# Performance work log

Measured on AMD Instinct MI355X. Metric: run time of the kernel, lower is better.

The kernel has to match this reference:

```python
import jax, jax.numpy as jnp
import numpy as np

BBOX_POS_MAX = 1024.0
BN_EPS = 1e-5


def _bn_eval(x, g, b, rm, rv):
    # BatchNorm1d in eval mode: affine transform with running stats
    return g * (x - rm) * jax.lax.rsqrt(rv + BN_EPS) + b


def setup_inputs() -> dict:
    key = jax.random.key(0)
    ks = jax.random.split(key, 24)
    B, N, F = 32, 512, 1024
    E = 32768
    H1, H2, H3 = 512, 256, 128          # node_pred_hidden
    EH1, EH2 = 64, 64                   # edge_pred_hidden
    NC, EC = 8, 10                      # node/edge concept channels
    BC = 9                              # bbox_channels (4 bbox + 4 dir + 1 prio)
    s = 0.02
    inp = {
        'roi_features': jax.random.normal(ks[0], (B, N, F), jnp.float32),
        'batch_bboxes': jax.random.uniform(ks[1], (B, N, 4), jnp.float32) * BBOX_POS_MAX,
        'batch_directions': jax.random.uniform(ks[2], (B, N, 4), jnp.float32),
        'batch_priorities': jax.random.uniform(ks[3], (B, N), jnp.float32),
        'batch_edge_index': jax.random.randint(ks[4], (B, 2, E), 0, N, jnp.int32),
        # node_predictor params
        'np_w1': jax.random.normal(ks[5], (F, H1), jnp.float32) * s,
        'np_b1': jnp.zeros((H1,), jnp.float32),
        'bn1_g': jnp.ones((H1,), jnp.float32),
        'bn1_b': jnp.zeros((H1,), jnp.float32),
        'bn1_rm': jnp.zeros((H1,), jnp.float32),
        'bn1_rv': jnp.ones((H1,), jnp.float32),
        'np_w2': jax.random.normal(ks[6], (H1, H2), jnp.float32) * s,
        'np_b2': jnp.zeros((H2,), jnp.float32),
        'bn2_g': jnp.ones((H2,), jnp.float32),
        'bn2_b': jnp.zeros((H2,), jnp.float32),
        'bn2_rm': jnp.zeros((H2,), jnp.float32),
        'bn2_rv': jnp.ones((H2,), jnp.float32),
        'np_w3': jax.random.normal(ks[7], (H2, H3), jnp.float32) * s,
        'np_b3': jnp.zeros((H3,), jnp.float32),
        'ni_w': jax.random.normal(ks[8], (H3, NC), jnp.float32) * s,
        'ni_b': jnp.zeros((NC,), jnp.float32),
        # edge_predictor params (input dim = 2 * bbox_channels)
        'ep_w1': jax.random.normal(ks[9], (2 * BC, EH1), jnp.float32) * s,
        'ep_b1': jnp.zeros((EH1,), jnp.float32),
        'ep_w2': jax.random.normal(ks[10], (EH1, EH2), jnp.float32) * s,
        'ep_b2': jnp.zeros((EH2,), jnp.float32),
        'ei_w': jax.random.normal(ks[11], (EH2, EC), jnp.float32) * s,
        'ei_b': jnp.zeros((EC,), jnp.float32),
    }
    return inp


def reference(roi_features, batch_bboxes, batch_directions, batch_priorities,
              batch_edge_index,
              np_w1, np_b1, bn1_g, bn1_b, bn1_rm, bn1_rv,
              np_w2, np_b2, bn2_g, bn2_b, bn2_rm, bn2_rv,
              np_w3, np_b3, ni_w, ni_b,
              ep_w1, ep_b1, ep_w2, ep_b2, ei_w, ei_b):
    B, N, F = roi_features.shape
    # ---- node path: MLP (eval-mode BN, dropout = identity) + sigmoid interpreter
    x = roi_features.reshape(B * N, F)
    h = jax.nn.relu(_bn_eval(x @ np_w1 + np_b1, bn1_g, bn1_b, bn1_rm, bn1_rv))
    h = jax.nn.relu(_bn_eval(h @ np_w2 + np_b2, bn2_g, bn2_b, bn2_rm, bn2_rv))
    h = jax.nn.relu(h @ np_w3 + np_b3)
    node_concepts = jax.nn.sigmoid(h @ ni_w + ni_b).reshape(B, N, -1)
    # ---- edge path: per-batch gather of node attrs via edge_index, concat, MLP
    node_attr = jnp.concatenate(
        [batch_bboxes / BBOX_POS_MAX, batch_directions, batch_priorities[..., None]],
        axis=-1)  # [B, N, 9]
    C = node_attr.shape[-1]
    src_idx = batch_edge_index[:, 0, :, None]  # [B, E, 1]
    dst_idx = batch_edge_index[:, 1, :, None]
    src = jnp.take_along_axis(node_attr, src_idx.astype(jnp.int32), axis=1)  # [B, E, 9]
    dst = jnp.take_along_axis(node_attr, dst_idx.astype(jnp.int32), axis=1)
    edge_attr = jnp.concatenate([src, dst], axis=-1).reshape(-1, 2 * C)  # [B*E, 18]
    e = jax.nn.relu(edge_attr @ ep_w1 + ep_b1)
    e = jax.nn.relu(e @ ep_w2 + ep_b2)
    edge_concepts = jax.nn.sigmoid(e @ ei_w + ei_b)  # [B*E, EC]
    return node_concepts, edge_concepts
```

## Files before the change

kernel.cpp:

```cpp
#include <hip/hip_runtime.h>
#include <cstdint>
#include <cstddef>

#define BN_EPSF 1e-5f

constexpr int B_  = 32, N_ = 512, F_ = 1024, E_ = 32768;
constexpr int H1_ = 512, H2_ = 256, H3_ = 128, NC_ = 8, EC_ = 10;
constexpr int M_  = B_ * N_;
constexpr int NE_ = B_ * E_;

typedef short bf16x8 __attribute__((ext_vector_type(8)));
typedef float f32x4  __attribute__((ext_vector_type(4)));

__device__ __forceinline__ short f2bf(float f) {
  union { float f; unsigned u; } v; v.f = f;
  unsigned r = v.u + 0x7fffu + ((v.u >> 16) & 1u);
  return (short)(r >> 16);
}
__device__ __forceinline__ unsigned cvtpk(float a, float b) {
  unsigned r;
  asm("v_cvt_pk_bf16_f32 %0, %1, %2" : "=v"(r) : "v"(a), "v"(b));
  return r;
}

#define GLDS(gp, lp) __builtin_amdgcn_global_load_lds( \
    (const __attribute__((address_space(1))) void*)(gp), \
    (__attribute__((address_space(3))) void*)(lp), 16, 0, 0)

#define MFMA(a, b, c) __builtin_amdgcn_mfma_f32_16x16x32_bf16((a), (b), (c), 0, 0, 0)

__device__ __forceinline__ void wt_body(
    const float* __restrict__ W, short* __restrict__ Wt, int K, int N,
    int bx, int by, float (*s)[33])
{
  const int tx = threadIdx.x & 31, ty = threadIdx.x >> 5;
  const int k0 = by * 32, n0 = bx * 32;
#pragma unroll
  for (int r = 0; r < 4; r++)
    s[ty * 4 + r][tx] = W[(size_t)(k0 + ty * 4 + r) * N + n0 + tx];
  __syncthreads();
#pragma unroll
  for (int r = 0; r < 4; r++)
    Wt[(size_t)(n0 + ty * 4 + r) * K + k0 + tx] = f2bf(s[tx][ty * 4 + r]);
}

__global__ __launch_bounds__(256) void k_prep(
    const float* __restrict__ roi, ushort* __restrict__ roiB,
    const float* __restrict__ w1, short* __restrict__ w1t,
    const float* __restrict__ w2, short* __restrict__ w2t,
    const float* __restrict__ w3, short* __restrict__ w3t)
{
  __shared__ float s[32][33];
  const int bx = blockIdx.x;
  if (bx < 8192) {
    int i = bx * 256 + threadIdx.x;
    float4 a = *(const float4*)(roi + (size_t)i * 8);
    float4 b = *(const float4*)(roi + (size_t)i * 8 + 4);
    unsigned o[4];
    o[0] = cvtpk(a.x, a.y); o[1] = cvtpk(a.z, a.w);
    o[2] = cvtpk(b.x, b.y); o[3] = cvtpk(b.z, b.w);
    *(uint4*)(roiB + (size_t)i * 8) = *(uint4*)o;
  } else if (bx < 8704) {
    int idx = bx - 8192; wt_body(w1, w1t, F_, H1_, idx & 15, idx >> 4, s);
  } else if (bx < 8832) {
    int idx = bx - 8704; wt_body(w2, w2t, H1_, H2_, idx & 7, idx >> 3, s);
  } else {
    int idx = bx - 8832; wt_body(w3, w3t, H2_, H3_, idx & 3, idx >> 2, s);
  }
}

__device__ __forceinline__ void relu_pack_shuf(
    const f32x4 (&acc)[4], int la, int lb, bool lo32, bf16x8 (&out)[2])
{
  unsigned plo[4], phi[4];
#pragma unroll
  for (int t = 0; t < 4; t++) {
    plo[t] = cvtpk(fmaxf(acc[t][0], 0.f), fmaxf(acc[t][1], 0.f));
    phi[t] = cvtpk(fmaxf(acc[t][2], 0.f), fmaxf(acc[t][3], 0.f));
  }
#pragma unroll
  for (int ks = 0; ks < 2; ks++) {
    unsigned w0a = (unsigned)__shfl((int)plo[2 * ks], la);
    unsigned w0b = (unsigned)__shfl((int)plo[2 * ks + 1], la);
    unsigned w1a = (unsigned)__shfl((int)phi[2 * ks], la);
    unsigned w1b = (unsigned)__shfl((int)phi[2 * ks + 1], la);
    unsigned w2a = (unsigned)__shfl((int)plo[2 * ks], lb);
    unsigned w2b = (unsigned)__shfl((int)plo[2 * ks + 1], lb);
    unsigned w3a = (unsigned)__shfl((int)phi[2 * ks], lb);
    unsigned w3b = (unsigned)__shfl((int)phi[2 * ks + 1], lb);
    union { unsigned u[4]; bf16x8 v; } t;
    t.u[0] = lo32 ? w0a : w0b;
    t.u[1] = lo32 ? w1a : w1b;
    t.u[2] = lo32 ? w2a : w2b;
    t.u[3] = lo32 ? w3a : w3b;
    out[ks] = t.v;
  }
}

__global__ __launch_bounds__(256, 3) void k_fused(
    const float* __restrict__ bbox, const float* __restrict__ dir,
    const float* __restrict__ pri, const int* __restrict__ eidx,
    const float* __restrict__ ew1, const float* __restrict__ eb1,
    const float* __restrict__ ew2, const float* __restrict__ eb2,
    const float* __restrict__ eow, const float* __restrict__ eob,
    float* __restrict__ out_edge,
    const short* __restrict__ roiB, const short* __restrict__ w1t,
    const float* __restrict__ b1, const float* __restrict__ g1,
    const float* __restrict__ bb1, const float* __restrict__ rm1,
    const float* __restrict__ rv1, short* __restrict__ h1)
{
  __shared__ __align__(16) char arena[38912];

  const int bx = blockIdx.x;
  const int rsel = bx % 3;
  const int tid  = threadIdx.x;
  const int wave = tid >> 6, lane = tid & 63;
  const int lm = lane & 15;

  if (rsel == 2) {
    const int lb = bx / 3;
    short* As = (short*)arena;
    short* Bs = (short*)(arena + 16384);
    const int m0 = (lb >> 2) * 128, n0 = (lb & 3) * 128;
    const int wm = wave >> 1, wn = wave & 1;
    const int q  = lane >> 4;
    const int srow = tid >> 3;
    const int sko  = ((tid & 7) ^ (srow & 7)) * 8;

    f32x4 acc[4][4] = {};
    for (int k0 = 0; k0 < F_; k0 += 64) {
#pragma unroll
      for (int it = 0; it < 4; it++)
        GLDS(roiB + (size_t)(m0 + it * 32 + srow) * F_ + k0 + sko,
             (char*)As + it * 4096 + wave * 1024);
#pragma unroll
      for (int it = 0; it < 4; it++)
        GLDS(w1t + (size_t)(n0 + it * 32 + srow) * F_ + k0 + sko,
             (char*)Bs + it * 4096 + wave * 1024);
      __syncthreads();

#pragma unroll
      for (int ks = 0; ks < 2; ks++) {
        const int co = (((ks * 4 + q) ^ (lm & 7)) * 8);
        bf16x8 af[4], bfr[4];
#pragma unroll
        for (int t = 0; t < 4; t++) {
          af[t]  = *(const bf16x8*)&As[(wm * 64 + t * 16 + lm) * 64 + co];
          bfr[t] = *(const bf16x8*)&Bs[(wn * 64 + t * 16 + lm) * 64 + co];
        }
#pragma unroll
        for (int ti = 0; ti < 4; ti++)
#pragma unroll
          for (int tj = 0; tj < 4; tj++)
            acc[ti][tj] = MFMA(af[ti], bfr[tj], acc[ti][tj]);
      }
      __syncthreads();
    }
#pragma unroll
    for (int tj = 0; tj < 4; tj++) {
      const int col = n0 + wn * 64 + tj * 16 + lm;
      const float bi = b1[col];
      float s = g1[col] * rsqrtf(rv1[col] + BN_EPSF);
      float t = bb1[col] - rm1[col] * s;
#pragma unroll
      for (int ti = 0; ti < 4; ti++) {
        const int rbase = m0 + wm * 64 + ti * 16 + ((lane >> 4) << 2);
#pragma unroll
        for (int r = 0; r < 4; r += 2) {
          float va = fmaf(acc[ti][tj][r]     + bi, s, t);
          float vb = fmaf(acc[ti][tj][r + 1] + bi, s, t);
          unsigned p = cvtpk(fmaxf(va, 0.f), fmaxf(vb, 0.f));
          h1[(size_t)(rbase + r)     * H1_ + col] = (short)p;
          h1[(size_t)(rbase + r + 1) * H1_ + col] = (short)(p >> 16);
        }
      }
    }
    return;
  }

  const int eb    = (bx / 3) * 2 + rsel;
  const int batch = eb >> 5;
  const int q     = lane >> 4;

  short*  sW1   = (short*)arena;
  short*  sW2   = (short*)(arena + 4096);
  short*  sW3   = (short*)(arena + 12288);
  ushort* sAttr = (ushort*)(arena + 14336);

  for (int i = tid; i < 2048; i += 256) {
    int n = i >> 5, k = i & 31;
    short v = 0;
    if (k < 9)                  v = f2bf(ew1[k * 64 + n]);
    else if (k >= 16 && k < 25) v = f2bf(ew1[(k - 7) * 64 + n]);
    sW1[i] = v;
  }
  for (int i = tid; i < 4096; i += 256) {
    int n = i >> 6, k = i & 63;
    sW2[i] = f2bf(ew2[k * 64 + n]);
  }
  for (int i = tid; i < 1024; i += 256) {
    int n = i >> 6, k = i & 63;
    sW3[i] = (n < 10) ? f2bf(eow[k * 10 + n]) : (short)0;
  }
  {
    const float inv = 1.0f / 1024.0f;
    for (int n = tid; n < 512; n += 256) {
      int gi = batch * 512 + n;
      float4 bv = *(const float4*)(bbox + (size_t)gi * 4);
      float4 dv = *(const float4*)(dir + (size_t)gi * 4);
      float pp = pri[gi];
      uint4 lo, hi;
      lo.x = cvtpk(bv.x * inv, bv.y * inv); lo.y = cvtpk(bv.z * inv, bv.w * inv);
      lo.z = cvtpk(dv.x, dv.y);             lo.w = cvtpk(dv.z, dv.w);
      hi.x = cvtpk(pp, 0.f); hi.y = 0; hi.z = 0; hi.w = 0;
      *(uint4*)&sAttr[n * 24]     = lo;
      *(uint4*)&sAttr[n * 24 + 8] = hi;
    }
  }
  __syncthreads();

  bf16x8 fW1[4], fW2[4][2], fW3[2];
#pragma unroll
  for (int t = 0; t < 4; t++)
    fW1[t] = *(const bf16x8*)&sW1[(t * 16 + lm) * 32 + q * 8];
#pragma unroll
  for (int t = 0; t < 4; t++)
#pragma unroll
    for (int ks = 0; ks < 2; ks++)
      fW2[t][ks] = *(const bf16x8*)&sW2[(t * 16 + lm) * 64 + ks * 32 + q * 8];
#pragma unroll
  for (int ks = 0; ks < 2; ks++)
    fW3[ks] = *(const bf16x8*)&sW3[lm * 64 + ks * 32 + q * 8];

  f32x4 b1q[4], b2q[4], boq;
#pragma unroll
  for (int t = 0; t < 4; t++) {
    b1q[t] = *(const f32x4*)(eb1 + t * 16 + q * 4);
    b2q[t] = *(const f32x4*)(eb2 + t * 16 + q * 4);
  }
#pragma unroll
  for (int r = 0; r < 4; r++)
    boq[r] = (q * 4 + r < 10) ? eob[q * 4 + r] : 0.f;

  const int  la   = (lane & 15) | ((lane & 16) << 1);
  const int  lbn  = la + 16;
  const bool lo32 = (lane < 32);
  const int* ip   = eidx + (size_t)batch * 2 * E_ + ((lane >= 32) ? E_ : 0);
  const int  ebl  = (eb & 31) * 1024;
  const int  ah   = (lane & 16) ? 8 : 0;

  int nidx[8][2];
#pragma unroll
  for (int b = 0; b < 8; b++)
#pragma unroll
    for (int ti = 0; ti < 2; ti++)
      nidx[b][ti] = ip[ebl + b * 128 + wave * 32 + ti * 16 + lm];

  bf16x8 xf[2];
#pragma unroll
  for (int ti = 0; ti < 2; ti++)
    xf[ti] = *(const bf16x8*)&sAttr[nidx[0][ti] * 24 + ah];

#pragma unroll
  for (int bi = 0; bi < 8; bi++) {
    bf16x8 xn[2];
    if (bi < 7) {
#pragma unroll
      for (int ti = 0; ti < 2; ti++)
        xn[ti] = *(const bf16x8*)&sAttr[nidx[bi + 1][ti] * 24 + ah];
    }

    f32x4 acc1[2][4];
#pragma unroll
    for (int tj = 0; tj < 4; tj++)
#pragma unroll
      for (int ti = 0; ti < 2; ti++)
        acc1[ti][tj] = MFMA(fW1[tj], xf[ti], b1q[tj]);
    bf16x8 xf2[2][2];
#pragma unroll
    for (int ti = 0; ti < 2; ti++)
      relu_pack_shuf(acc1[ti], la, lbn, lo32, xf2[ti]);

    f32x4 acc2[2][4];
#pragma unroll
    for (int ti = 0; ti < 2; ti++)
#pragma unroll
      for (int tj = 0; tj < 4; tj++)
        acc2[ti][tj] = b2q[tj];
#pragma unroll
    for (int ks = 0; ks < 2; ks++)
#pragma unroll
      for (int tj = 0; tj < 4; tj++)
#pragma unroll
        for (int ti = 0; ti < 2; ti++)
          acc2[ti][tj] = MFMA(fW2[tj][ks], xf2[ti][ks], acc2[ti][tj]);
    bf16x8 xf3[2][2];
#pragma unroll
    for (int ti = 0; ti < 2; ti++)
      relu_pack_shuf(acc2[ti], la, lbn, lo32, xf3[ti]);

#pragma unroll
    for (int ti = 0; ti < 2; ti++) {
      f32x4 a3 = boq;
#pragma unroll
      for (int ks = 0; ks < 2; ks++)
        a3 = MFMA(fW3[ks], xf3[ti][ks], a3);
      float o[4];
#pragma unroll
      for (int r = 0; r < 4; r++)
        o[r] = 1.f / (1.f + __expf(-a3[r]));
      size_t base = (size_t)(eb * 1024 + bi * 128 + wave * 32 + ti * 16 + lm) * 10;
      if (q == 0) {
        float2 t0; t0.x = o[0]; t0.y = o[1]; *(float2*)(out_edge + base)     = t0;
        float2 t1; t1.x = o[2]; t1.y = o[3]; *(float2*)(out_edge + base + 2) = t1;
      } else if (q == 1) {
        float2 t0; t0.x = o[0]; t0.y = o[1]; *(float2*)(out_edge + base + 4) = t0;
        float2 t1; t1.x = o[2]; t1.y = o[3]; *(float2*)(out_edge + base + 6) = t1;
      } else if (q == 2) {
        float2 t0; t0.x = o[0]; t0.y = o[1]; *(float2*)(out_edge + base + 8) = t0;
      }
    }
    xf[0] = xn[0]; xf[1] = xn[1];
  }
}

__global__ __launch_bounds__(256) void k_tail(
    const short* __restrict__ h1, const short* __restrict__ w2t,
    const short* __restrict__ w3t,
    const float* __restrict__ b2, const float* __restrict__ g2,
    const float* __restrict__ bb2, const float* __restrict__ rm2,
    const float* __restrict__ rv2,
    const float* __restrict__ b3, const float* __restrict__ niw,
    const float* __restrict__ nib, float* __restrict__ out)
{
  __shared__ __align__(16) char arena[53760];
  short* sA  = (short*)arena;
  short* sB  = (short*)(arena + 4096);
  short* sH2 = (short*)(arena + 36864);
  short* sB3 = (short*)arena;
  short* sH3 = (short*)(arena + 16384);

  const int tid  = threadIdx.x;
  const int wave = tid >> 6, lane = tid & 63;
  const int lm = lane & 15, q = lane >> 4;
  const int wm = wave >> 1, wn = wave & 1;
  const int m0 = blockIdx.x * 32;
  const int srow = tid >> 2;
  const int skq  = ((tid & 3) ^ ((tid >> 3) & 3)) * 8;
  const int sq   = (q ^ ((lm >> 1) & 3)) * 8;

  f32x4 acc2[8] = {};
  for (int k0 = 0; k0 < 512; k0 += 64) {
    {
      int c = tid >> 7, row = (tid >> 2) & 31;
      GLDS(h1 + (size_t)(m0 + row) * 512 + k0 + c * 32 + skq,
           (char*)sA + wave * 1024);
    }
#pragma unroll
    for (int it = 0; it < 4; it++)
#pragma unroll
      for (int c = 0; c < 2; c++)
        GLDS(w2t + (size_t)(it * 64 + srow) * 512 + k0 + c * 32 + skq,
             (char*)sB + c * 16384 + it * 4096 + wave * 1024);
    __syncthreads();
#pragma unroll
    for (int c = 0; c < 2; c++) {
      bf16x8 af = *(const bf16x8*)&sA[c * 1024 + (wm * 16 + lm) * 32 + sq];
#pragma unroll
      for (int nt = 0; nt < 8; nt++) {
        bf16x8 bfr = *(const bf16x8*)&sB[c * 8192 + (wn * 128 + nt * 16 + lm) * 32 + sq];
        acc2[nt] = MFMA(af, bfr, acc2[nt]);
      }
    }
    __syncthreads();
  }
#pragma unroll
  for (int nt = 0; nt < 8; nt++) {
    int col = wn * 128 + nt * 16 + lm;
    float s = g2[col] * rsqrtf(rv2[col] + BN_EPSF);
    float t = bb2[col] - rm2[col] * s;
    float bi = b2[col];
    float v0 = fmaf(acc2[nt][0] + bi, s, t);
    float v1 = fmaf(acc2[nt][1] + bi, s, t);
    float v2 = fmaf(acc2[nt][2] + bi, s, t);
    float v3 = fmaf(acc2[nt][3] + bi, s, t);
    unsigned p01 = cvtpk(fmaxf(v0, 0.f), fmaxf(v1, 0.f));
    unsigned p23 = cvtpk(fmaxf(v2, 0.f), fmaxf(v3, 0.f));
    int rb = wm * 16 + q * 4;
    sH2[(rb + 0) * 264 + col] = (short)p01;
    sH2[(rb + 1) * 264 + col] = (short)(p01 >> 16);
    sH2[(rb + 2) * 264 + col] = (short)p23;
    sH2[(rb + 3) * 264 + col] = (short)(p23 >> 16);
  }
  __syncthreads();

  f32x4 acc3[4] = {};
  for (int k0 = 0; k0 < 256; k0 += 64) {
#pragma unroll
    for (int it = 0; it < 2; it++)
#pragma unroll
      for (int c = 0; c < 2; c++)
        GLDS(w3t + (size_t)(it * 64 + srow) * 256 + k0 + c * 32 + skq,
             (char*)sB3 + c * 8192 + it * 4096 + wave * 1024);
    __syncthreads();
#pragma unroll
    for (int c = 0; c < 2; c++) {
      bf16x8 af = *(const bf16x8*)&sH2[(wm * 16 + lm) * 264 + k0 + c * 32 + q * 8];
#pragma unroll
      for (int nt = 0; nt < 4; nt++) {
        bf16x8 bfr = *(const bf16x8*)&sB3[c * 4096 + (wn * 64 + nt * 16 + lm) * 32 + sq];
        acc3[nt] = MFMA(af, bfr, acc3[nt]);
      }
    }
    __syncthreads();
  }
#pragma unroll
  for (int nt = 0; nt < 4; nt++) {
    int col = wn * 64 + nt * 16 + lm;
    float bi = b3[col];
    float v0 = acc3[nt][0] + bi;
    float v1 = acc3[nt][1] + bi;
    float v2 = acc3[nt][2] + bi;
    float v3 = acc3[nt][3] + bi;
    unsigned p01 = cvtpk(fmaxf(v0, 0.f), fmaxf(v1, 0.f));
    unsigned p23 = cvtpk(fmaxf(v2, 0.f), fmaxf(v3, 0.f));
    int rb = wm * 16 + q * 4;
    sH3[(rb + 0) * 136 + col] = (short)p01;
    sH3[(rb + 1) * 136 + col] = (short)(p01 >> 16);
    sH3[(rb + 2) * 136 + col] = (short)p23;
    sH3[(rb + 3) * 136 + col] = (short)(p23 >> 16);
  }
  __syncthreads();

  if (wave < 2) {
    f32x4 a4 = {};
#pragma unroll
    for (int c = 0; c < 4; c++) {
      ushort tmp[8];
#pragma unroll
      for (int j = 0; j < 8; j++) {
        int k = c * 32 + q * 8 + j;
        tmp[j] = (lm < 8) ? (ushort)f2bf(niw[k * 8 + lm]) : (ushort)0;
      }
      bf16x8 fw = *(bf16x8*)tmp;
      bf16x8 af4 = *(const bf16x8*)&sH3[(wave * 16 + lm) * 136 + c * 32 + q * 8];
      a4 = MFMA(af4, fw, a4);
    }
    if (lm < 8) {
      float bi = nib[lm];
#pragma unroll
      for (int r = 0; r < 4; r++) {
        float v = a4[r] + bi;
        out[(size_t)(m0 + wave * 16 + q * 4 + r) * 8 + lm] = 1.f / (1.f + __expf(-v));
      }
    }
  }
}

extern "C" void kernel_launch(void* const* d_in, const int* in_sizes, int n_in,
                              void* d_out, int out_size, void* d_ws, size_t ws_size,
                              hipStream_t stream)
{
  const float* roi   = (const float*)d_in[0];
  const float* bbox  = (const float*)d_in[1];
  const float* dir   = (const float*)d_in[2];
  const float* pri   = (const float*)d_in[3];
  const int*   eidx  = (const int*)d_in[4];
  const float* w1    = (const float*)d_in[5];
  const float* b1    = (const float*)d_in[6];
  const float* g1    = (const float*)d_in[7];
  const float* bb1   = (const float*)d_in[8];
  const float* rm1   = (const float*)d_in[9];
  const float* rv1   = (const float*)d_in[10];
  const float* w2    = (const float*)d_in[11];
  const float* b2    = (const float*)d_in[12];
  const float* g2    = (const float*)d_in[13];
  const float* bb2   = (const float*)d_in[14];
  const float* rm2   = (const float*)d_in[15];
  const float* rv2   = (const float*)d_in[16];
  const float* w3    = (const float*)d_in[17];
  const float* b3    = (const float*)d_in[18];
  const float* niw   = (const float*)d_in[19];
  const float* nib   = (const float*)d_in[20];
  const float* ew1   = (const float*)d_in[21];
  const float* eb1   = (const float*)d_in[22];
  const float* ew2   = (const float*)d_in[23];
  const float* eb2   = (const float*)d_in[24];
  const float* eow   = (const float*)d_in[25];
  const float* eob   = (const float*)d_in[26];

  float* out_node = (float*)d_out;
  float* out_edge = (float*)d_out + (size_t)M_ * NC_;

  char* w = (char*)d_ws;
  short*  roiB = (short*)w;
  short*  w1t  = (short*)(w + 33554432);
  short*  w2t  = (short*)(w + 34603008);
  short*  w3t  = (short*)(w + 34865152);
  short*  h1   = (short*)(w + 35717120);

  k_prep<<<8864, 256, 0, stream>>>(roi, (ushort*)roiB, w1, w1t, w2, w2t,
                                   w3, w3t);

  k_fused<<<1536, 256, 0, stream>>>(
      bbox, dir, pri, eidx, ew1, eb1, ew2, eb2, eow, eob, out_edge,
      roiB, w1t, b1, g1, bb1, rm1, rv1, h1);

  k_tail<<<M_ / 32, 256, 0, stream>>>(
      h1, w2t, w3t, b2, g2, bb2, rm2, rv2, b3, niw, nib, out_node);
}
```

Measured before the change: 237.9 us.

## Precompute bf16 node attrs in prep and double-buffer tail GEMM staging

Node attribute packing (bbox scaling, directions, priority to bf16) moves from every edge block into the prep kernel, which writes a global table. Edge blocks now gather the attributes straight from global memory instead of staging them in LDS, which shrinks their LDS footprint. The tail kernel's layer-2 and layer-3 GEMMs switch to double-buffered LDS staging so the next K-tile loads overlap the current MFMAs. The cost is more LDS in the tail kernel (72KB), which may reduce its occupancy, and edge gathers that now go to global/L2 instead of LDS.

Measured after the change: 239.4 us. About the same (+0.6%).

```diff
diff --git a/kernel.cpp b/kernel.cpp
--- a/kernel.cpp
+++ b/kernel.cpp
@@ -48,7 +48,9 @@
     const float* __restrict__ roi, ushort* __restrict__ roiB,
     const float* __restrict__ w1, short* __restrict__ w1t,
     const float* __restrict__ w2, short* __restrict__ w2t,
-    const float* __restrict__ w3, short* __restrict__ w3t)
+    const float* __restrict__ w3, short* __restrict__ w3t,
+    const float* __restrict__ bbox, const float* __restrict__ dir,
+    const float* __restrict__ pri, ushort* __restrict__ attrT)
 {
   __shared__ float s[32][33];
   const int bx = blockIdx.x;
@@ -64,8 +66,20 @@
     int idx = bx - 8192; wt_body(w1, w1t, F_, H1_, idx & 15, idx >> 4, s);
   } else if (bx < 8832) {
     int idx = bx - 8704; wt_body(w2, w2t, H1_, H2_, idx & 7, idx >> 3, s);
+  } else if (bx < 8864) {
+    int idx = bx - 8832; wt_body(w3, w3t, H2_, H3_, idx & 3, idx >> 2, s);
   } else {
-    int idx = bx - 8832; wt_body(w3, w3t, H2_, H3_, idx & 3, idx >> 2, s);
+    int gi = (bx - 8864) * 256 + threadIdx.x;
+    const float inv = 1.0f / 1024.0f;
+    float4 bv = *(const float4*)(bbox + (size_t)gi * 4);
+    float4 dv = *(const float4*)(dir + (size_t)gi * 4);
+    float pp = pri[gi];
+    uint4 lo, hi;
+    lo.x = cvtpk(bv.x * inv, bv.y * inv); lo.y = cvtpk(bv.z * inv, bv.w * inv);
+    lo.z = cvtpk(dv.x, dv.y);             lo.w = cvtpk(dv.z, dv.w);
+    hi.x = cvtpk(pp, 0.f); hi.y = 0; hi.z = 0; hi.w = 0;
+    *(uint4*)(attrT + (size_t)gi * 16)     = lo;
+    *(uint4*)(attrT + (size_t)gi * 16 + 8) = hi;
   }
 }
 
@@ -98,8 +112,7 @@
 }
 
 __global__ __launch_bounds__(256, 3) void k_fused(
-    const float* __restrict__ bbox, const float* __restrict__ dir,
-    const float* __restrict__ pri, const int* __restrict__ eidx,
+    const ushort* __restrict__ attrT, const int* __restrict__ eidx,
     const float* __restrict__ ew1, const float* __restrict__ eb1,
     const float* __restrict__ ew2, const float* __restrict__ eb2,
     const float* __restrict__ eow, const float* __restrict__ eob,
@@ -109,7 +122,7 @@
     const float* __restrict__ bb1, const float* __restrict__ rm1,
     const float* __restrict__ rv1, short* __restrict__ h1)
 {
-  __shared__ __align__(16) char arena[38912];
+  __shared__ __align__(16) char arena[32768];
 
   const int bx = blockIdx.x;
   const int rsel = bx % 3;
@@ -185,7 +198,6 @@
   short*  sW1   = (short*)arena;
   short*  sW2   = (short*)(arena + 4096);
   short*  sW3   = (short*)(arena + 12288);
-  ushort* sAttr = (ushort*)(arena + 14336);
 
   for (int i = tid; i < 2048; i += 256) {
     int n = i >> 5, k = i & 31;
@@ -202,21 +214,6 @@
     int n = i >> 6, k = i & 63;
     sW3[i] = (n < 10) ? f2bf(eow[k * 10 + n]) : (short)0;
   }
-  {
-    const float inv = 1.0f / 1024.0f;
-    for (int n = tid; n < 512; n += 256) {
-      int gi = batch * 512 + n;
-      float4 bv = *(const float4*)(bbox + (size_t)gi * 4);
-      float4 dv = *(const float4*)(dir + (size_t)gi * 4);
-      float pp = pri[gi];
-      uint4 lo, hi;
-      lo.x = cvtpk(bv.x * inv, bv.y * inv); lo.y = cvtpk(bv.z * inv, bv.w * inv);
-      lo.z = cvtpk(dv.x, dv.y);             lo.w = cvtpk(dv.z, dv.w);
-      hi.x = cvtpk(pp, 0.f); hi.y = 0; hi.z = 0; hi.w = 0;
-      *(uint4*)&sAttr[n * 24]     = lo;
-      *(uint4*)&sAttr[n * 24 + 8] = hi;
-    }
-  }
   __syncthreads();
 
   bf16x8 fW1[4], fW2[4][2], fW3[2];
@@ -248,6 +245,7 @@
   const int* ip   = eidx + (size_t)batch * 2 * E_ + ((lane >= 32) ? E_ : 0);
   const int  ebl  = (eb & 31) * 1024;
   const int  ah   = (lane & 16) ? 8 : 0;
+  const ushort* atb = attrT + (size_t)batch * 512 * 16 + ah;
 
   int nidx[8][2];
 #pragma unroll
@@ -259,7 +257,7 @@
   bf16x8 xf[2];
 #pragma unroll
   for (int ti = 0; ti < 2; ti++)
-    xf[ti] = *(const bf16x8*)&sAttr[nidx[0][ti] * 24 + ah];
+    xf[ti] = *(const bf16x8*)(atb + nidx[0][ti] * 16);
 
 #pragma unroll
   for (int bi = 0; bi < 8; bi++) {
@@ -267,7 +265,7 @@
     if (bi < 7) {
 #pragma unroll
       for (int ti = 0; ti < 2; ti++)
-        xn[ti] = *(const bf16x8*)&sAttr[nidx[bi + 1][ti] * 24 + ah];
+        xn[ti] = *(const bf16x8*)(atb + nidx[bi + 1][ti] * 16);
     }
 
     f32x4 acc1[2][4];
@@ -324,6 +322,51 @@
   }
 }
 
+#define STAGE_A(bufA, bufB, k0) do {                                        \
+    { int c_ = tid >> 7, row_ = (tid >> 2) & 31;                            \
+      GLDS(h1 + (size_t)(m0 + row_) * 512 + (k0) + c_ * 32 + skq,           \
+           (char*)(bufA) + wave * 1024); }                                  \
+    _Pragma("unroll")                                                       \
+    for (int it = 0; it < 4; it++)                                          \
+      _Pragma("unroll")                                                     \
+      for (int c = 0; c < 2; c++)                                           \
+        GLDS(w2t + (size_t)(it * 64 + srow) * 512 + (k0) + c * 32 + skq,    \
+             (char*)(bufB) + c * 16384 + it * 4096 + wave * 1024);          \
+  } while (0)
+
+#define COMP_A(bufA, bufB) do {                                             \
+    _Pragma("unroll")                                                       \
+    for (int c = 0; c < 2; c++) {                                           \
+      bf16x8 af = *(const bf16x8*)&((const short*)(bufA))                   \
+          [c * 1024 + (wm * 16 + lm) * 32 + sq];                            \
+      _Pragma("unroll")                                                     \
+      for (int nt = 0; nt < 8; nt++) {                                      \
+        bf16x8 bfr = *(const bf16x8*)&((const short*)(bufB))                \
+            [c * 8192 + (wn * 128 + nt * 16 + lm) * 32 + sq];               \
+        acc2[nt] = MFMA(af, bfr, acc2[nt]);                                 \
+      } } } while (0)
+
+#define STAGE_B(bufB, k0) do {                                              \
+    _Pragma("unroll")                                                       \
+    for (int it = 0; it < 2; it++)                                          \
+      _Pragma("unroll")                                                     \
+      for (int c = 0; c < 2; c++)                                           \
+        GLDS(w3t + (size_t)(it * 64 + srow) * 256 + (k0) + c * 32 + skq,    \
+             (char*)(bufB) + c * 8192 + it * 4096 + wave * 1024);           \
+  } while (0)
+
+#define COMP_B(bufB, k0) do {                                               \
+    _Pragma("unroll")                                                       \
+    for (int c = 0; c < 2; c++) {                                           \
+      bf16x8 af = *(const bf16x8*)&sH2[(wm * 16 + lm) * 264                 \
+          + (k0) + c * 32 + q * 8];                                         \
+      _Pragma("unroll")                                                     \
+      for (int nt = 0; nt < 4; nt++) {                                      \
+        bf16x8 bfr = *(const bf16x8*)&((const short*)(bufB))                \
+            [c * 4096 + (wn * 64 + nt * 16 + lm) * 32 + sq];                \
+        acc3[nt] = MFMA(af, bfr, acc3[nt]);                                 \
+      } } } while (0)
+
 __global__ __launch_bounds__(256) void k_tail(
     const short* __restrict__ h1, const short* __restrict__ w2t,
     const short* __restrict__ w3t,
@@ -333,12 +376,12 @@
     const float* __restrict__ b3, const float* __restrict__ niw,
     const float* __restrict__ nib, float* __restrict__ out)
 {
-  __shared__ __align__(16) char arena[53760];
-  short* sA  = (short*)arena;
-  short* sB  = (short*)(arena + 4096);
-  short* sH2 = (short*)(arena + 36864);
-  short* sB3 = (short*)arena;
-  short* sH3 = (short*)(arena + 16384);
+  __shared__ __align__(16) char arena[73728];
+  char* const A0 = arena;          char* const A1 = arena + 4096;
+  char* const Bb0 = arena + 8192;  char* const Bb1 = arena + 40960;
+  char* const B3a = arena + 20480; char* const B3b = arena + 36864;
+  short* sH2 = (short*)arena;
+  short* sH3 = (short*)(arena + 53248);
 
   const int tid  = threadIdx.x;
   const int wave = tid >> 6, lane = tid & 63;
@@ -350,28 +393,15 @@
   const int sq   = (q ^ ((lm >> 1) & 3)) * 8;
 
   f32x4 acc2[8] = {};
-  for (int k0 = 0; k0 < 512; k0 += 64) {
-    {
-      int c = tid >> 7, row = (tid >> 2) & 31;
-      GLDS(h1 + (size_t)(m0 + row) * 512 + k0 + c * 32 + skq,
-           (char*)sA + wave * 1024);
-    }
-#pragma unroll
-    for (int it = 0; it < 4; it++)
-#pragma unroll
-      for (int c = 0; c < 2; c++)
-        GLDS(w2t + (size_t)(it * 64 + srow) * 512 + k0 + c * 32 + skq,
-             (char*)sB + c * 16384 + it * 4096 + wave * 1024);
+  STAGE_A(A0, Bb0, 0);
+  __syncthreads();
+#pragma unroll
+  for (int t = 0; t < 8; t += 2) {
+    if (t + 1 < 8) STAGE_A(A1, Bb1, (t + 1) * 64);
+    COMP_A(A0, Bb0);
     __syncthreads();
-#pragma unroll
-    for (int c = 0; c < 2; c++) {
-      bf16x8 af = *(const bf16x8*)&sA[c * 1024 + (wm * 16 + lm) * 32 + sq];
-#pragma unroll
-      for (int nt = 0; nt < 8; nt++) {
-        bf16x8 bfr = *(const bf16x8*)&sB[c * 8192 + (wn * 128 + nt * 16 + lm) * 32 + sq];
-        acc2[nt] = MFMA(af, bfr, acc2[nt]);
-      }
-    }
+    if (t + 2 < 8) STAGE_A(A0, Bb0, (t + 2) * 64);
+    COMP_A(A1, Bb1);
     __syncthreads();
   }
 #pragma unroll
@@ -392,26 +422,17 @@
     sH2[(rb + 2) * 264 + col] = (short)p23;
     sH2[(rb + 3) * 264 + col] = (short)(p23 >> 16);
   }
+  STAGE_B(B3a, 0);
   __syncthreads();
 
   f32x4 acc3[4] = {};
-  for (int k0 = 0; k0 < 256; k0 += 64) {
-#pragma unroll
-    for (int it = 0; it < 2; it++)
-#pragma unroll
-      for (int c = 0; c < 2; c++)
-        GLDS(w3t + (size_t)(it * 64 + srow) * 256 + k0 + c * 32 + skq,
-             (char*)sB3 + c * 8192 + it * 4096 + wave * 1024);
+#pragma unroll
+  for (int t = 0; t < 4; t += 2) {
+    if (t + 1 < 4) STAGE_B(B3b, (t + 1) * 64);
+    COMP_B(B3a, t * 64);
     __syncthreads();
-#pragma unroll
-    for (int c = 0; c < 2; c++) {
-      bf16x8 af = *(const bf16x8*)&sH2[(wm * 16 + lm) * 264 + k0 + c * 32 + q * 8];
-#pragma unroll
-      for (int nt = 0; nt < 4; nt++) {
-        bf16x8 bfr = *(const bf16x8*)&sB3[c * 4096 + (wn * 64 + nt * 16 + lm) * 32 + sq];
-        acc3[nt] = MFMA(af, bfr, acc3[nt]);
-      }
-    }
+    if (t + 2 < 4) STAGE_B(B3a, (t + 2) * 64);
+    COMP_B(B3b, (t + 1) * 64);
     __syncthreads();
   }
 #pragma unroll
@@ -493,17 +514,18 @@
   float* out_edge = (float*)d_out + (size_t)M_ * NC_;
 
   char* w = (char*)d_ws;
-  short*  roiB = (short*)w;
-  short*  w1t  = (short*)(w + 33554432);
-  short*  w2t  = (short*)(w + 34603008);
-  short*  w3t  = (short*)(w + 34865152);
-  short*  h1   = (short*)(w + 35717120);
-
-  k_prep<<<8864, 256, 0, stream>>>(roi, (ushort*)roiB, w1, w1t, w2, w2t,
-                                   w3, w3t);
+  short*  roiB  = (short*)w;
+  short*  w1t   = (short*)(w + 33554432);
+  short*  w2t   = (short*)(w + 34603008);
+  short*  w3t   = (short*)(w + 34865152);
+  ushort* attrT = (ushort*)(w + 34930688);
+  short*  h1    = (short*)(w + 35717120);
+
+  k_prep<<<8928, 256, 0, stream>>>(roi, (ushort*)roiB, w1, w1t, w2, w2t,
+                                   w3, w3t, bbox, dir, pri, attrT);
 
   k_fused<<<1536, 256, 0, stream>>>(
-      bbox, dir, pri, eidx, ew1, eb1, ew2, eb2, eow, eob, out_edge,
+      attrT, eidx, ew1, eb1, ew2, eb2, eow, eob, out_edge,
       roiB, w1t, b1, g1, bb1, rm1, rv1, h1);
 
   k_tail<<<M_ / 32, 256, 0, stream>>>(
```
